# Kernel optimization log

Measured on AMD Instinct MI355X. Metric: run time of the kernel, lower is better.

The kernel has to match this reference:

```python
import jax, jax.numpy as jnp
import numpy as np

B_SZ, SEQ = 16, 2048
VOCAB, EMBED = 50257, 128
DSTATE, HID, NCLS = 16, 256, 10
NEDGE = 8192  # edges per graph (avg degree 4)
LN_EPS = 1e-5


def setup_inputs() -> dict:
    key = jax.random.key(0)
    ks = jax.random.split(key, 12)
    tokens = jax.random.randint(ks[0], (B_SZ, SEQ), 0, VOCAB, dtype=jnp.int32)
    lengths = jnp.full((B_SZ,), SEQ, dtype=jnp.int32)  # full-length graphs
    edge_indices = jax.random.randint(ks[1], (B_SZ, 2, NEDGE), 0, SEQ, dtype=jnp.int32)
    emb = (jax.random.normal(ks[2], (VOCAB, EMBED)) * 0.02).at[0].set(0.0)  # padding_idx=0
    A_log = jax.random.normal(ks[3], (EMBED, DSTATE)) * 0.1
    B_w = jax.random.normal(ks[4], (DSTATE, EMBED)) * (1.0 / np.sqrt(EMBED))
    C_w = jax.random.normal(ks[5], (EMBED, DSTATE)) * (1.0 / np.sqrt(DSTATE))
    D_skip = jnp.ones((EMBED,))
    ln_g = jnp.ones((EMBED,))
    ln_b = jnp.zeros((EMBED,))
    Wmsg_w = jax.random.normal(ks[6], (HID, EMBED)) * (1.0 / np.sqrt(EMBED))
    Wupd_w = jax.random.normal(ks[7], (HID, EMBED + HID)) * (1.0 / np.sqrt(EMBED + HID))
    Wupd_b = jax.random.normal(ks[8], (HID,)) * 0.01
    cls_w = jax.random.normal(ks[9], (NCLS, HID)) * (1.0 / np.sqrt(HID))
    cls_b = jnp.zeros((NCLS,))
    return {"tokens": tokens, "lengths": lengths, "edge_indices": edge_indices,
            "emb": emb, "A_log": A_log, "B_w": B_w, "C_w": C_w, "D_skip": D_skip,
            "ln_g": ln_g, "ln_b": ln_b, "Wmsg_w": Wmsg_w, "Wupd_w": Wupd_w,
            "Wupd_b": Wupd_b, "cls_w": cls_w, "cls_b": cls_b}


def _ssm(x, A_log, B_w, C_w, D_skip, ln_g, ln_b):
    # x: (B, S, d_model). Diagonal SSM: h_t = h_{t-1}*exp(A) + B x_t (broadcast over d_model)
    Aexp = jnp.exp(-jnp.exp(A_log))  # (d_model, d_state)
    h0 = jnp.zeros((x.shape[0], EMBED, DSTATE), dtype=x.dtype)

    def step(h, x_t):  # x_t: (B, d_model)
        b_t = x_t @ B_w.T                            # (B, d_state)
        h = h * Aexp[None] + b_t[:, None, :]          # (B, d_model, d_state)
        y = h.mean(axis=1) @ C_w.T + D_skip * x_t     # (B, d_model)
        return h, y

    _, ys = jax.lax.scan(step, h0, jnp.swapaxes(x, 0, 1))
    out = jnp.swapaxes(ys, 0, 1)                      # (B, S, d_model)
    mu = out.mean(-1, keepdims=True)
    var = jnp.mean((out - mu) ** 2, axis=-1, keepdims=True)
    return ln_g * (out - mu) * jax.lax.rsqrt(var + LN_EPS) + ln_b


def reference(tokens, lengths, edge_indices, emb, A_log, B_w, C_w, D_skip,
              ln_g, ln_b, Wmsg_w, Wupd_w, Wupd_b, cls_w, cls_b):
    x = emb[tokens]                                   # (B, S, E)
    h = _ssm(x, A_log, B_w, C_w, D_skip, ln_g, ln_b)  # (B, S, E)
    src, dst = edge_indices[:, 0, :], edge_indices[:, 1, :]   # (B, Ne)
    h_src = jnp.take_along_axis(h, src[:, :, None], axis=1)   # (B, Ne, E)
    msgs = jnp.einsum('bed,hd->beh', h_src, Wmsg_w)            # (B, Ne, H)
    flat_dst = (jnp.arange(B_SZ, dtype=dst.dtype)[:, None] * SEQ + dst).reshape(-1)
    agg = jax.ops.segment_sum(msgs.reshape(-1, HID), flat_dst,
                              num_segments=B_SZ * SEQ).reshape(B_SZ, SEQ, HID)
    upd = jax.nn.relu(jnp.concatenate([h, agg], axis=-1) @ Wupd_w.T + Wupd_b)  # (B, S, H)
    pooled = upd.mean(axis=1)                          # (B, H)  (all lengths == SEQ)
    return pooled @ cls_w.T + cls_b                    # (B, NCLS)
```

## Files before the change

### kernel.cpp

```cpp
#include <hip/hip_runtime.h>

#define B_SZ   16
#define SEQ    2048
#define VOCAB  50257
#define EMBED  128
#define DSTATE 16
#define HID    256
#define NCLS   10
#define NEDGE  8192
#define KTR    64
#define LN_EPS 1e-5f
#define NROW   (B_SZ*SEQ)
#define BCAP   32
#define OVCAP  1024

#define PB_CAST   4096
#define PB_BUCKET (PB_CAST + 512)
#define PB_PRECM  (PB_BUCKET + 128)
#define PB_CTAB   (PB_PRECM + 16)
#define PB_TOTAL  (PB_CTAB + 1)

typedef float  f32x4 __attribute__((ext_vector_type(4)));
typedef short  s16x8 __attribute__((ext_vector_type(8)));

__device__ __forceinline__ float scrub(float x){
  return (x == x && fabsf(x) < 1e30f) ? x : 0.f;
}
__device__ __forceinline__ short f2b(float f){
  unsigned int u = __float_as_uint(f);
  unsigned int r = (u + 0x7fffu + ((u >> 16) & 1u)) >> 16;
  return (short)r;
}
__device__ __forceinline__ unsigned int pack2(float a, float b){
  return (unsigned int)(unsigned short)f2b(a)
       | ((unsigned int)(unsigned short)f2b(b) << 16);
}
__device__ __forceinline__ float lo2f(unsigned int v){ return __uint_as_float(v << 16); }
__device__ __forceinline__ float hi2f(unsigned int v){ return __uint_as_float(v & 0xffff0000u); }

__global__ __launch_bounds__(256) void k_prep(
    const int* __restrict__ tokens, const float* __restrict__ emb,
    const float* __restrict__ A_log, const float* __restrict__ B_w,
    const float* __restrict__ Wmsg, const float* __restrict__ Wupd,
    const int* __restrict__ edges,
    float* __restrict__ c_tab, short* __restrict__ Bf, float* __restrict__ MT,
    unsigned int* __restrict__ x_bf, int* __restrict__ cnt,
    unsigned short* __restrict__ bucket, int* __restrict__ ovf_cnt,
    int* __restrict__ ovf){
  int bid = blockIdx.x, tid = threadIdx.x;
  if (bid < PB_CAST){
    int gid = bid*256 + tid;
    int row = gid >> 5, ch = gid & 31;
    int tok = tokens[row];
    tok = tok < 0 ? 0 : (tok >= VOCAB ? VOCAB-1 : tok);
    float4 v = *(const float4*)(emb + (size_t)tok*EMBED + ch*4);
    uint2 o; o.x = pack2(v.x, v.y); o.y = pack2(v.z, v.w);
    *(uint2*)(x_bf + (size_t)row*(EMBED/2) + ch*2) = o;
  } else if (bid < PB_BUCKET){
    int eid = (bid-PB_CAST)*256 + tid;
    int b = eid >> 13, i = eid & (NEDGE-1);
    const int* ei = edges + (size_t)b*2*NEDGE;
    int s = ei[i]         & (SEQ-1);
    int d = ei[NEDGE + i] & (SEQ-1);
    int gdst = (b << 11) | d;
    int slot = atomicAdd(&cnt[gdst], 1);
    if (slot < BCAP) bucket[(size_t)gdst*BCAP + slot] = (unsigned short)s;
    else {
      int o = atomicAdd(ovf_cnt, 1);
      if (o < OVCAP) ovf[o] = ((b << 11) | s) | (gdst << 16);
    }
  } else if (bid < PB_PRECM){
    int hp = (bid-PB_BUCKET)*2 + (tid >> 7);
    int e  = tid & 127;
    const float* w2 = Wupd + (size_t)hp*384 + 128;
    float acc = 0.f;
    for (int h1 = 0; h1 < HID; ++h1)
      acc += Wmsg[h1*EMBED + e] * w2[h1];
    MT[(size_t)hp*EMBED + e] = scrub(acc);
  } else if (bid < PB_CTAB){
    if (tid < 64){
      int d = bid - PB_PRECM, lane = tid;
      float a0 = scrub(expf(-expf(A_log[(2*lane+0)*DSTATE + d])));
      float a1 = scrub(expf(-expf(A_log[(2*lane+1)*DSTATE + d])));
      float p0 = 1.f, p1 = 1.f;
      for (int k = 0; k < KTR; ++k){
        float s = p0 + p1;
        for (int off = 32; off; off >>= 1) s += __shfl_down(s, off);
        if (lane == 0) c_tab[k*DSTATE + d] = scrub(s * (1.0f/128.0f));
        p0 *= a0; p1 *= a1;
      }
    }
  } else {
    int idx = tid;
    int c = idx >> 6, lane = idx & 63;
    int n = lane & 15;
    int kb = c*32 + (lane >> 4)*8;
    short v[8];
    #pragma unroll
    for (int jj = 0; jj < 8; ++jj) v[jj] = f2b(B_w[(size_t)n*EMBED + kb + jj]);
    *(s16x8*)(Bf + (size_t)idx*8) = *(s16x8*)v;
  }
}

__global__ __launch_bounds__(256) void k_ssm_fused(
    const short* __restrict__ x_bf, const float* __restrict__ c_tab,
    const float* __restrict__ C_w, const float* __restrict__ D_skip,
    const float* __restrict__ ln_g, const float* __restrict__ ln_b,
    const short* __restrict__ Bf, const float* __restrict__ Wupd,
    const float* __restrict__ MT, unsigned int* __restrict__ h_out,
    short* __restrict__ Wcs){
  __shared__ float bsh[128][18];
  __shared__ float msh[64][18];
  __shared__ float Ct[DSTATE][EMBED+2];
  __shared__ float csh[KTR][DSTATE];
  int bid = blockIdx.x, tid = threadIdx.x;

  if (bid >= 512){
    int idx = (bid-512)*256 + tid;
    int c    = idx >> 10;
    int rem  = idx & 1023;
    int j    = rem >> 6;
    int lane = rem & 63;
    int n  = j*16 + (lane & 15);
    int kb = c*32 + (lane >> 4)*8;
    short v[8];
    #pragma unroll
    for (int jj = 0; jj < 8; ++jj){
      int k = kb + jj;
      float val = (k < 128) ? Wupd[(size_t)n*384 + k] : MT[(size_t)n*EMBED + (k-128)];
      v[jj] = f2b(val);
    }
    *(s16x8*)(Wcs + (size_t)idx*8) = *(s16x8*)v;
    return;
  }

  int b  = bid >> 5;
  int t0 = (bid & 31) * 64;
  for (int i = tid; i < DSTATE*EMBED; i += 256){
    int e = i >> 4, d = i & 15;
    Ct[d][e] = C_w[i];
  }
  for (int i = tid; i < KTR*DSTATE; i += 256)
    csh[i >> 4][i & 15] = c_tab[i];

  int wv = tid >> 6, lane = tid & 63;
  int m = lane & 15, lg = lane >> 4;

  const s16x8* Bp = (const s16x8*)Bf;
  #pragma unroll
  for (int tt = 0; tt < 2; ++tt){
    int tile = wv*2 + tt;
    int trow = t0 - 64 + tile*16;
    f32x4 acc = (f32x4){0.f,0.f,0.f,0.f};
    if (trow >= 0){
      const short* xrow = x_bf + ((size_t)(b*SEQ + trow + m))*EMBED + lg*8;
      #pragma unroll
      for (int c = 0; c < 4; ++c){
        s16x8 a = *(const s16x8*)(xrow + c*32);
        acc = __builtin_amdgcn_mfma_f32_16x16x32_bf16(a, Bp[c*64 + lane], acc, 0, 0, 0);
      }
    }
    #pragma unroll
    for (int r = 0; r < 4; ++r)
      bsh[tile*16 + lg*4 + r][m] = scrub(acc[r]);
  }
  __syncthreads();

  {
    int d  = tid & 15;
    int qb = (tid >> 4) * 4;
    float a0=0.f, a1=0.f, a2=0.f, a3=0.f;
    float w0 = bsh[64+qb+0][d];
    float w1 = bsh[64+qb+1][d];
    float w2 = bsh[64+qb+2][d];
    float w3 = bsh[64+qb+3][d];
    #pragma unroll
    for (int k = 0; k < KTR; ++k){
      float c = csh[k][d];
      a0 += c*w0; a1 += c*w1; a2 += c*w2; a3 += c*w3;
      w3 = w2; w2 = w1; w1 = w0;
      w0 = (k+1 < KTR) ? bsh[64+qb-k-1][d] : 0.f;
    }
    msh[qb+0][d] = scrub(a0); msh[qb+1][d] = scrub(a1);
    msh[qb+2][d] = scrub(a2); msh[qb+3][d] = scrub(a3);
  }
  __syncthreads();

  int e0 = lane*2;
  float2 dsk = *(const float2*)&D_skip[e0];
  float2 lgv = *(const float2*)&ln_g[e0];
  float2 lbv = *(const float2*)&ln_b[e0];
  const unsigned int* xb = (const unsigned int*)x_bf;
  for (int q = wv*16; q < wv*16+16; ++q){
    int row = b*SEQ + t0 + q;
    unsigned int xp = xb[(size_t)row*(EMBED/2) + lane];
    float x0 = lo2f(xp), x1 = hi2f(xp);
    float y0 = dsk.x*x0, y1 = dsk.y*x1;
    #pragma unroll
    for (int d = 0; d < DSTATE; ++d){
      float md = msh[q][d];
      y0 += md * Ct[d][e0];
      y1 += md * Ct[d][e0+1];
    }
    y0 = scrub(y0); y1 = scrub(y1);
    float s = y0+y1, s2 = y0*y0 + y1*y1;
    for (int off = 32; off; off >>= 1){ s += __shfl_down(s,off); s2 += __shfl_down(s2,off); }
    s = __shfl(s, 0); s2 = __shfl(s2, 0);
    float mu  = s * (1.f/EMBED);
    float var = s2 * (1.f/EMBED) - mu*mu;
    float inv = rsqrtf(fmaxf(var, 0.f) + LN_EPS);
    float o0 = scrub(lgv.x*(y0-mu)*inv + lbv.x);
    float o1 = scrub(lgv.y*(y1-mu)*inv + lbv.y);
    h_out[(size_t)row*(EMBED/2) + lane] = pack2(o0, o1);
  }
}

__global__ __launch_bounds__(256) void k_upd_fused(
    const short* __restrict__ h, const int* __restrict__ cnt,
    const unsigned short* __restrict__ bucket,
    const int* __restrict__ ovf_cnt, const int* __restrict__ ovf,
    const short* __restrict__ Wcs, const float* __restrict__ Wupd_b,
    float* __restrict__ pool, int* __restrict__ done,
    const float* __restrict__ cls_w, const float* __restrict__ cls_b,
    float* __restrict__ out){
  __shared__ float psum[4][HID];
  __shared__ float plds[B_SZ*HID];
  __shared__ int   lastflag;
  int tid  = threadIdx.x;
  int wv   = tid >> 6, lane = tid & 63;
  int wave = blockIdx.x*4 + wv;
  int row0 = wave * 16;
  int b    = row0 >> 11;
  int m = lane & 15, lg = lane >> 4;
  int r = row0 + m;

  const short* hrow = h + (size_t)r*EMBED + lg*8;
  s16x8 hfrag[4];
  #pragma unroll
  for (int c = 0; c < 4; ++c) hfrag[c] = *(const s16x8*)(hrow + c*32);

  float ge[32];
  #pragma unroll
  for (int i = 0; i < 32; ++i) ge[i] = 0.f;
  int n = cnt[r]; n = n > BCAP ? BCAP : n;
  const unsigned short* bk = bucket + (size_t)r*BCAP;
  const short* hb = h + ((size_t)(b << 11))*EMBED;
  for (int i = 0; i < n; ++i){
    int s = bk[i];
    const short* hs = hb + (size_t)s*EMBED + lg*8;
    #pragma unroll
    for (int c = 0; c < 4; ++c){
      uint4 p = *(const uint4*)(hs + c*32);
      ge[c*8+0] += lo2f(p.x); ge[c*8+1] += hi2f(p.x);
      ge[c*8+2] += lo2f(p.y); ge[c*8+3] += hi2f(p.y);
      ge[c*8+4] += lo2f(p.z); ge[c*8+5] += hi2f(p.z);
      ge[c*8+6] += lo2f(p.w); ge[c*8+7] += hi2f(p.w);
    }
  }
  int on = *ovf_cnt; on = on > OVCAP ? OVCAP : on;
  for (int idx = 0; idx < on; ++idx){
    int pk = ovf[idx];
    if (((pk >> 16) & 0x7fff) == r){
      const short* hs = h + (size_t)(pk & 0xffff)*EMBED + lg*8;
      #pragma unroll
      for (int c = 0; c < 4; ++c){
        uint4 p = *(const uint4*)(hs + c*32);
        ge[c*8+0] += lo2f(p.x); ge[c*8+1] += hi2f(p.x);
        ge[c*8+2] += lo2f(p.y); ge[c*8+3] += hi2f(p.y);
        ge[c*8+4] += lo2f(p.z); ge[c*8+5] += hi2f(p.z);
        ge[c*8+6] += lo2f(p.w); ge[c*8+7] += hi2f(p.w);
      }
    }
  }
  s16x8 gfrag[4];
  #pragma unroll
  for (int c = 0; c < 4; ++c){
    short v[8];
    #pragma unroll
    for (int j = 0; j < 8; ++j) v[j] = f2b(scrub(ge[c*8+j]));
    gfrag[c] = *(s16x8*)v;
  }

  f32x4 acc[16];
  #pragma unroll
  for (int j = 0; j < 16; ++j) acc[j] = (f32x4){0.f,0.f,0.f,0.f};
  const s16x8* Bp = (const s16x8*)Wcs;
  #pragma unroll
  for (int c = 0; c < 8; ++c){
    s16x8 a = (c < 4) ? hfrag[c] : gfrag[c-4];
    #pragma unroll
    for (int j = 0; j < 16; ++j){
      s16x8 bfr = Bp[(c*16 + j)*64 + lane];
      acc[j] = __builtin_amdgcn_mfma_f32_16x16x32_bf16(a, bfr, acc[j], 0, 0, 0);
    }
  }

  #pragma unroll
  for (int j = 0; j < 16; ++j){
    int nn = j*16 + m;
    float bias = Wupd_b[nn];
    float v = 0.f;
    #pragma unroll
    for (int rr = 0; rr < 4; ++rr) v += fmaxf(acc[j][rr] + bias, 0.f);
    v += __shfl_down(v, 32);
    v += __shfl_down(v, 16);
    if (lane < 16) psum[wv][nn] = scrub(v);
  }
  __syncthreads();
  if (tid < HID){
    float t = psum[0][tid] + psum[1][tid] + psum[2][tid] + psum[3][tid];
    atomicAdd(&pool[b*HID + tid], t);
  }
  __threadfence();
  __syncthreads();
  if (tid == 0){
    int prev = atomicAdd(done, 1);
    lastflag = (prev == (int)gridDim.x - 1);
  }
  __syncthreads();
  if (!lastflag) return;

  for (int i = tid; i < B_SZ*HID; i += 256)
    plds[i] = __hip_atomic_load(&pool[i], __ATOMIC_RELAXED, __HIP_MEMORY_SCOPE_AGENT);
  __syncthreads();
  if (tid < B_SZ*NCLS){
    int bb = tid / NCLS, c = tid - bb*NCLS;
    const float* w = cls_w + c*HID;
    float s = 0.f;
    for (int h1 = 0; h1 < HID; ++h1) s += plds[bb*HID + h1] * w[h1];
    out[tid] = scrub(s * (1.0f/SEQ) + cls_b[c]);
  }
}

extern "C" void kernel_launch(void* const* d_in, const int* in_sizes, int n_in,
                              void* d_out, int out_size, void* d_ws, size_t ws_size,
                              hipStream_t stream) {
  const int*   tokens = (const int*)d_in[0];
  const int*   edges  = (const int*)d_in[2];
  const float* emb    = (const float*)d_in[3];
  const float* A_log  = (const float*)d_in[4];
  const float* B_w    = (const float*)d_in[5];
  const float* C_w    = (const float*)d_in[6];
  const float* D_skip = (const float*)d_in[7];
  const float* ln_g   = (const float*)d_in[8];
  const float* ln_b   = (const float*)d_in[9];
  const float* Wmsg   = (const float*)d_in[10];
  const float* Wupd   = (const float*)d_in[11];
  const float* Wupd_b = (const float*)d_in[12];
  const float* cls_w  = (const float*)d_in[13];
  const float* cls_b  = (const float*)d_in[14];
  float* out = (float*)d_out;

  char* ws = (char*)d_ws;
  float* c_tab = (float*)ws;  ws += 16*1024;
  float* MT    = (float*)ws;  ws += (size_t)HID*EMBED*4;
  short* Wcs   = (short*)ws;  ws += (size_t)HID*HID*2;
  short* Bf    = (short*)ws;  ws += 16*1024;
  char*  zbase = ws;
  float* pool  = (float*)ws;  ws += (size_t)B_SZ*HID*4;
  int*   cnt   = (int*)ws;    ws += (size_t)NROW*4;
  int*   ovf_cnt = (int*)ws;  ws += 64;
  int*   done  = (int*)ws;    ws += 64;
  int*   ovf   = (int*)ws;    ws += OVCAP*4;
  size_t zlen = (size_t)((char*)ws - zbase);
  unsigned short* bucket = (unsigned short*)ws; ws += (size_t)NROW*BCAP*2;
  short* x_bf  = (short*)ws;  ws += (size_t)NROW*EMBED*2;
  short* h_bf  = (short*)ws;  ws += (size_t)NROW*EMBED*2;

  hipMemsetAsync(zbase, 0, zlen, stream);
  hipLaunchKernelGGL(k_prep, dim3(PB_TOTAL), dim3(256), 0, stream,
                     tokens, emb, A_log, B_w, Wmsg, Wupd, edges,
                     c_tab, Bf, MT, (unsigned int*)x_bf, cnt, bucket, ovf_cnt, ovf);
  hipLaunchKernelGGL(k_ssm_fused, dim3(544), dim3(256), 0, stream,
                     x_bf, c_tab, C_w, D_skip, ln_g, ln_b, Bf, Wupd, MT,
                     (unsigned int*)h_bf, Wcs);
  hipLaunchKernelGGL(k_upd_fused, dim3(NROW/64), dim3(256), 0, stream,
                     h_bf, cnt, bucket, ovf_cnt, ovf, Wcs, Wupd_b,
                     pool, done, cls_w, cls_b, out);
}
```

Before: 201.8 us.

## Repartition SSM and update kernels across more blocks with per-wave row gathers

The SSM kernel now uses 512-thread blocks that each cover 32 timesteps instead of 64, with one thread per (q,d) convolution output, doubling the grid. The update kernel gives each block 16 rows. Each wave gathers neighbour sums for 4 rows with coalesced 32-bit loads into shared memory, and the four waves split the 256 output columns. Pool partials go straight to global atomics. The aim is more parallelism and lower register pressure, at the cost of more redundant halo work in the SSM kernel and more atomics and blocks in the update kernel.

```diff
diff --git a/kernel.cpp b/kernel.cpp
--- a/kernel.cpp
+++ b/kernel.cpp
@@ -102,21 +102,21 @@
   }
 }
 
-__global__ __launch_bounds__(256) void k_ssm_fused(
+__global__ __launch_bounds__(512, 8) void k_ssm_fused(
     const short* __restrict__ x_bf, const float* __restrict__ c_tab,
     const float* __restrict__ C_w, const float* __restrict__ D_skip,
     const float* __restrict__ ln_g, const float* __restrict__ ln_b,
     const short* __restrict__ Bf, const float* __restrict__ Wupd,
     const float* __restrict__ MT, unsigned int* __restrict__ h_out,
     short* __restrict__ Wcs){
-  __shared__ float bsh[128][18];
-  __shared__ float msh[64][18];
+  __shared__ float bsh[96][18];
+  __shared__ float msh[32][18];
   __shared__ float Ct[DSTATE][EMBED+2];
   __shared__ float csh[KTR][DSTATE];
   int bid = blockIdx.x, tid = threadIdx.x;
 
-  if (bid >= 512){
-    int idx = (bid-512)*256 + tid;
+  if (bid >= 1024){
+    int idx = (bid-1024)*512 + tid;
     int c    = idx >> 10;
     int rem  = idx & 1023;
     int j    = rem >> 6;
@@ -134,22 +134,21 @@
     return;
   }
 
-  int b  = bid >> 5;
-  int t0 = (bid & 31) * 64;
-  for (int i = tid; i < DSTATE*EMBED; i += 256){
+  int b  = bid >> 6;
+  int t0 = (bid & 63) * 32;
+  for (int i = tid; i < DSTATE*EMBED; i += 512){
     int e = i >> 4, d = i & 15;
     Ct[d][e] = C_w[i];
   }
-  for (int i = tid; i < KTR*DSTATE; i += 256)
+  for (int i = tid; i < KTR*DSTATE; i += 512)
     csh[i >> 4][i & 15] = c_tab[i];
 
   int wv = tid >> 6, lane = tid & 63;
   int m = lane & 15, lg = lane >> 4;
 
   const s16x8* Bp = (const s16x8*)Bf;
-  #pragma unroll
-  for (int tt = 0; tt < 2; ++tt){
-    int tile = wv*2 + tt;
+  if (wv < 6){
+    int tile = wv;
     int trow = t0 - 64 + tile*16;
     f32x4 acc = (f32x4){0.f,0.f,0.f,0.f};
     if (trow >= 0){
@@ -167,22 +166,13 @@
   __syncthreads();
 
   {
-    int d  = tid & 15;
-    int qb = (tid >> 4) * 4;
-    float a0=0.f, a1=0.f, a2=0.f, a3=0.f;
-    float w0 = bsh[64+qb+0][d];
-    float w1 = bsh[64+qb+1][d];
-    float w2 = bsh[64+qb+2][d];
-    float w3 = bsh[64+qb+3][d];
-    #pragma unroll
-    for (int k = 0; k < KTR; ++k){
-      float c = csh[k][d];
-      a0 += c*w0; a1 += c*w1; a2 += c*w2; a3 += c*w3;
-      w3 = w2; w2 = w1; w1 = w0;
-      w0 = (k+1 < KTR) ? bsh[64+qb-k-1][d] : 0.f;
-    }
-    msh[qb+0][d] = scrub(a0); msh[qb+1][d] = scrub(a1);
-    msh[qb+2][d] = scrub(a2); msh[qb+3][d] = scrub(a3);
+    int d = tid & 15;
+    int q = tid >> 4;
+    float acc = 0.f;
+    #pragma unroll
+    for (int k = 0; k < KTR; ++k)
+      acc += csh[k][d] * bsh[64 + q - k][d];
+    msh[q][d] = scrub(acc);
   }
   __syncthreads();
 
@@ -191,7 +181,7 @@
   float2 lgv = *(const float2*)&ln_g[e0];
   float2 lbv = *(const float2*)&ln_b[e0];
   const unsigned int* xb = (const unsigned int*)x_bf;
-  for (int q = wv*16; q < wv*16+16; ++q){
+  for (int q = wv*4; q < wv*4+4; ++q){
     int row = b*SEQ + t0 + q;
     unsigned int xp = xb[(size_t)row*(EMBED/2) + lane];
     float x0 = lo2f(xp), x1 = hi2f(xp);
@@ -215,7 +205,7 @@
   }
 }
 
-__global__ __launch_bounds__(256) void k_upd_fused(
+__global__ __launch_bounds__(256, 6) void k_upd_fused(
     const short* __restrict__ h, const int* __restrict__ cnt,
     const unsigned short* __restrict__ bucket,
     const int* __restrict__ ovf_cnt, const int* __restrict__ ovf,
@@ -223,93 +213,71 @@
     float* __restrict__ pool, int* __restrict__ done,
     const float* __restrict__ cls_w, const float* __restrict__ cls_b,
     float* __restrict__ out){
-  __shared__ float psum[4][HID];
-  __shared__ float plds[B_SZ*HID];
-  __shared__ int   lastflag;
+  __shared__ unsigned int smem[B_SZ*HID];
+  __shared__ int lastflag;
   int tid  = threadIdx.x;
   int wv   = tid >> 6, lane = tid & 63;
-  int wave = blockIdx.x*4 + wv;
-  int row0 = wave * 16;
+  int row0 = blockIdx.x * 16;
   int b    = row0 >> 11;
   int m = lane & 15, lg = lane >> 4;
-  int r = row0 + m;
-
-  const short* hrow = h + (size_t)r*EMBED + lg*8;
-  s16x8 hfrag[4];
-  #pragma unroll
-  for (int c = 0; c < 4; ++c) hfrag[c] = *(const s16x8*)(hrow + c*32);
-
-  float ge[32];
-  #pragma unroll
-  for (int i = 0; i < 32; ++i) ge[i] = 0.f;
-  int n = cnt[r]; n = n > BCAP ? BCAP : n;
-  const unsigned short* bk = bucket + (size_t)r*BCAP;
-  const short* hb = h + ((size_t)(b << 11))*EMBED;
-  for (int i = 0; i < n; ++i){
-    int s = bk[i];
-    const short* hs = hb + (size_t)s*EMBED + lg*8;
-    #pragma unroll
-    for (int c = 0; c < 4; ++c){
-      uint4 p = *(const uint4*)(hs + c*32);
-      ge[c*8+0] += lo2f(p.x); ge[c*8+1] += hi2f(p.x);
-      ge[c*8+2] += lo2f(p.y); ge[c*8+3] += hi2f(p.y);
-      ge[c*8+4] += lo2f(p.z); ge[c*8+5] += hi2f(p.z);
-      ge[c*8+6] += lo2f(p.w); ge[c*8+7] += hi2f(p.w);
-    }
-  }
+
+  const unsigned int* hb32 = (const unsigned int*)h + (size_t)(b*SEQ)*(EMBED/2);
+  const unsigned int* h32  = (const unsigned int*)h;
   int on = *ovf_cnt; on = on > OVCAP ? OVCAP : on;
-  for (int idx = 0; idx < on; ++idx){
-    int pk = ovf[idx];
-    if (((pk >> 16) & 0x7fff) == r){
-      const short* hs = h + (size_t)(pk & 0xffff)*EMBED + lg*8;
-      #pragma unroll
-      for (int c = 0; c < 4; ++c){
-        uint4 p = *(const uint4*)(hs + c*32);
-        ge[c*8+0] += lo2f(p.x); ge[c*8+1] += hi2f(p.x);
-        ge[c*8+2] += lo2f(p.y); ge[c*8+3] += hi2f(p.y);
-        ge[c*8+4] += lo2f(p.z); ge[c*8+5] += hi2f(p.z);
-        ge[c*8+6] += lo2f(p.w); ge[c*8+7] += hi2f(p.w);
+  for (int i = 0; i < 4; ++i){
+    int rloc = wv*4 + i;
+    int r = row0 + rloc;
+    int n = cnt[r]; n = n > BCAP ? BCAP : n;
+    const unsigned short* bk = bucket + (size_t)r*BCAP;
+    float ax = 0.f, ay = 0.f;
+    for (int t = 0; t < n; ++t){
+      unsigned int v = hb32[(size_t)bk[t]*(EMBED/2) + lane];
+      ax += lo2f(v); ay += hi2f(v);
+    }
+    for (int idx = 0; idx < on; ++idx){
+      int pk = ovf[idx];
+      if (((pk >> 16) & 0x7fff) == r){
+        unsigned int v = h32[(size_t)(pk & 0xffff)*(EMBED/2) + lane];
+        ax += lo2f(v); ay += hi2f(v);
       }
     }
-  }
-  s16x8 gfrag[4];
+    smem[rloc*68 + lane] = pack2(scrub(ax), scrub(ay));
+  }
+  __syncthreads();
+
+  const short* hrow = h + (size_t)(row0+m)*EMBED + lg*8;
+  s16x8 hfrag[4], gfrag[4];
   #pragma unroll
   for (int c = 0; c < 4; ++c){
-    short v[8];
-    #pragma unroll
-    for (int j = 0; j < 8; ++j) v[j] = f2b(scrub(ge[c*8+j]));
-    gfrag[c] = *(s16x8*)v;
-  }
-
-  f32x4 acc[16];
+    hfrag[c] = *(const s16x8*)(hrow + c*32);
+    gfrag[c] = *(const s16x8*)&smem[m*68 + c*16 + lg*4];
+  }
+
+  int j0 = wv*4;
+  f32x4 acc[4];
   #pragma unroll
-  for (int j = 0; j < 16; ++j) acc[j] = (f32x4){0.f,0.f,0.f,0.f};
+  for (int jj = 0; jj < 4; ++jj) acc[jj] = (f32x4){0.f,0.f,0.f,0.f};
   const s16x8* Bp = (const s16x8*)Wcs;
   #pragma unroll
   for (int c = 0; c < 8; ++c){
     s16x8 a = (c < 4) ? hfrag[c] : gfrag[c-4];
     #pragma unroll
-    for (int j = 0; j < 16; ++j){
-      s16x8 bfr = Bp[(c*16 + j)*64 + lane];
-      acc[j] = __builtin_amdgcn_mfma_f32_16x16x32_bf16(a, bfr, acc[j], 0, 0, 0);
+    for (int jj = 0; jj < 4; ++jj){
+      s16x8 bfr = Bp[(c*16 + j0 + jj)*64 + lane];
+      acc[jj] = __builtin_amdgcn_mfma_f32_16x16x32_bf16(a, bfr, acc[jj], 0, 0, 0);
     }
   }
 
   #pragma unroll
-  for (int j = 0; j < 16; ++j){
-    int nn = j*16 + m;
+  for (int jj = 0; jj < 4; ++jj){
+    int nn = (j0 + jj)*16 + m;
     float bias = Wupd_b[nn];
     float v = 0.f;
     #pragma unroll
-    for (int rr = 0; rr < 4; ++rr) v += fmaxf(acc[j][rr] + bias, 0.f);
+    for (int rr = 0; rr < 4; ++rr) v += fmaxf(acc[jj][rr] + bias, 0.f);
     v += __shfl_down(v, 32);
     v += __shfl_down(v, 16);
-    if (lane < 16) psum[wv][nn] = scrub(v);
-  }
-  __syncthreads();
-  if (tid < HID){
-    float t = psum[0][tid] + psum[1][tid] + psum[2][tid] + psum[3][tid];
-    atomicAdd(&pool[b*HID + tid], t);
+    if (lane < 16) atomicAdd(&pool[b*HID + nn], scrub(v));
   }
   __threadfence();
   __syncthreads();
@@ -320,6 +288,7 @@
   __syncthreads();
   if (!lastflag) return;
 
+  float* plds = (float*)smem;
   for (int i = tid; i < B_SZ*HID; i += 256)
     plds[i] = __hip_atomic_load(&pool[i], __ATOMIC_RELAXED, __HIP_MEMORY_SCOPE_AGENT);
   __syncthreads();
@@ -371,10 +340,10 @@
   hipLaunchKernelGGL(k_prep, dim3(PB_TOTAL), dim3(256), 0, stream,
                      tokens, emb, A_log, B_w, Wmsg, Wupd, edges,
                      c_tab, Bf, MT, (unsigned int*)x_bf, cnt, bucket, ovf_cnt, ovf);
-  hipLaunchKernelGGL(k_ssm_fused, dim3(544), dim3(256), 0, stream,
+  hipLaunchKernelGGL(k_ssm_fused, dim3(1040), dim3(512), 0, stream,
                      x_bf, c_tab, C_w, D_skip, ln_g, ln_b, Bf, Wupd, MT,
                      (unsigned int*)h_bf, Wcs);
-  hipLaunchKernelGGL(k_upd_fused, dim3(NROW/64), dim3(256), 0, stream,
+  hipLaunchKernelGGL(k_upd_fused, dim3(NROW/16), dim3(256), 0, stream,
                      h_bf, cnt, bucket, ovf_cnt, ovf, Wcs, Wupd_b,
                      pool, done, cls_w, cls_b, out);
 }
```

New measurement: 369.5 us. 1.83x slower.
